# Optimization experiments

Measured on AMD Instinct MI355X. Metric: run time of the kernel, lower is better.

## Reference

```python
import jax, jax.numpy as jnp
import numpy as np

B, S, DIM = 32, 1, 4096
N_HEADS, N_KV, HD = 32, 8, 128
N_REP = N_HEADS // N_KV
MAX_SEQ = 2048


def _rope(x, cos, sin):
    # x: [b, s, h, d]; cos/sin: [s, d//2]; rotate consecutive pairs
    x2 = x.reshape(*x.shape[:-1], HD // 2, 2)
    x0, x1 = x2[..., 0], x2[..., 1]
    c = cos[None, :, None, :]
    s = sin[None, :, None, :]
    o0 = x0 * c - x1 * s
    o1 = x0 * s + x1 * c
    return jnp.stack([o0, o1], axis=-1).reshape(x.shape)


def setup_inputs() -> dict:
    key = jax.random.key(0)
    ks = jax.random.split(key, 9)
    start_pos = 2047
    # true RoPE frequencies at position start_pos
    inv_freq = 1.0 / (10000.0 ** (np.arange(0, HD, 2, dtype=np.float32) / HD))
    ang = (start_pos * inv_freq).astype(np.float32)[None, :]  # [1, HD//2]
    return {
        "x": jax.random.normal(ks[0], (B, S, DIM), jnp.float32),
        "freqs_cos": jnp.asarray(np.cos(ang)),
        "freqs_sin": jnp.asarray(np.sin(ang)),
        "wq": jax.random.normal(ks[1], (DIM, DIM), jnp.float32) * 0.02,
        "wk": jax.random.normal(ks[2], (N_KV * HD, DIM), jnp.float32) * 0.02,
        "wv": jax.random.normal(ks[3], (N_KV * HD, DIM), jnp.float32) * 0.02,
        "wo": jax.random.normal(ks[4], (DIM, DIM), jnp.float32) * 0.02,
        "cache_k": jax.random.normal(ks[5], (B, MAX_SEQ, N_KV, HD), jnp.float32),
        "cache_v": jax.random.normal(ks[6], (B, MAX_SEQ, N_KV, HD), jnp.float32),
        "start_pos": start_pos,
    }


def reference(x, freqs_cos, freqs_sin, wq, wk, wv, wo, cache_k, cache_v, start_pos):
    b, s, dim = x.shape  # s == 1 (decode)
    xq = (x @ wq.T).reshape(b, s, N_HEADS, HD)
    xk = (x @ wk.T).reshape(b, s, N_KV, HD)
    xv = (x @ wv.T).reshape(b, s, N_KV, HD)
    xq = _rope(xq, freqs_cos, freqs_sin)
    xk = _rope(xk, freqs_cos, freqs_sin)
    # KV-cache scatter write at start_pos
    cache_k = jax.lax.dynamic_update_slice(cache_k, xk, (0, start_pos, 0, 0))
    cache_v = jax.lax.dynamic_update_slice(cache_v, xv, (0, start_pos, 0, 0))
    t = start_pos + s
    keys = cache_k[:, :t]    # [b, t, kv, hd]
    values = cache_v[:, :t]  # [b, t, kv, hd]
    # GQA: group query heads over kv heads (no repeat_kv materialization)
    q = xq[:, 0].reshape(b, N_KV, N_REP, HD)  # [b, kv, rep, hd]
    scale = HD ** -0.5
    attn = jnp.einsum("bkrd,btkd->bkrt", q, keys) * scale  # [b, kv, rep, t]
    attn = jax.nn.softmax(attn.astype(jnp.float32), axis=-1).astype(q.dtype)
    out = jnp.einsum("bkrt,btkd->bkrd", attn, values).reshape(b, s, dim)
    return out @ wo.T
```

## Files before the change

kernel.cpp:

```cpp
#include <hip/hip_runtime.h>
#include <math.h>

#define B_ 32
#define DIM_ 4096
#define NKV_ 8
#define HD_ 128
#define T_ 2048
#define KS_ 16
#define QKV_ROWS_ 6144
#define O_ROWS_ 4096
#define NCHUNK_ 16
#define NSPLITW_ 64

#define Q_OFF    0
#define KNEW_OFF (Q_OFF + B_*DIM_)
#define VNEW_OFF (KNEW_OFF + B_*NKV_*HD_)
#define AO_OFF   (VNEW_OFF + B_*NKV_*HD_)
#define PQKV_OFF (AO_OFF + B_*DIM_)
#define PO_OFF   (PQKV_OFF + KS_*QKV_ROWS_*B_)
#define OPART_OFF (PO_OFF + KS_*O_ROWS_*B_)
#define ML_OFF   (OPART_OFF + B_*NKV_*NSPLITW_*4*HD_)

__device__ __forceinline__ void fma4(float4& a, const float4& x, float w) {
    a.x = fmaf(x.x, w, a.x); a.y = fmaf(x.y, w, a.y);
    a.z = fmaf(x.z, w, a.z); a.w = fmaf(x.w, w, a.w);
}

template<int NROWS>
__global__ __launch_bounds__(256) void gemm_split(
    const float* __restrict__ X, const float* __restrict__ W0,
    const float* __restrict__ W1, const float* __restrict__ W2,
    float* __restrict__ part)
{
    __shared__ float xs[32][36];
    __shared__ float wsh[32][132];
    const int rb = blockIdx.x, ks = blockIdx.y;
    const int row0 = rb * 128;
    const float* W; int wr0;
    if (NROWS == 4096 || row0 < 4096) { W = W0; wr0 = row0; }
    else if (row0 < 5120)             { W = W1; wr0 = row0 - 4096; }
    else                              { W = W2; wr0 = row0 - 5120; }
    const int tid = threadIdx.x;
    const int rt = tid & 31, bt = tid >> 5;
    float4 acc[4];
    acc[0] = acc[1] = acc[2] = acc[3] = make_float4(0.f,0.f,0.f,0.f);
    const int kc0 = ks * 256;
    const int xb = tid >> 3, xkq = tid & 7;
    float4 xpf, wpf[4];
    xpf = *(const float4*)(X + xb * DIM_ + kc0 + xkq * 4);
    #pragma unroll
    for (int j = 0; j < 4; ++j)
        wpf[j] = *(const float4*)(W + (wr0 + xb + 32*j) * DIM_ + kc0 + xkq * 4);
    for (int kt = 0; kt < 8; ++kt) {
        __syncthreads();
        xs[xkq*4+0][xb] = xpf.x; xs[xkq*4+1][xb] = xpf.y;
        xs[xkq*4+2][xb] = xpf.z; xs[xkq*4+3][xb] = xpf.w;
        #pragma unroll
        for (int j = 0; j < 4; ++j) {
            const int r = xb + 32*j;
            wsh[xkq*4+0][r] = wpf[j].x; wsh[xkq*4+1][r] = wpf[j].y;
            wsh[xkq*4+2][r] = wpf[j].z; wsh[xkq*4+3][r] = wpf[j].w;
        }
        __syncthreads();
        if (kt < 7) {
            const int kc = kc0 + (kt + 1) * 32;
            xpf = *(const float4*)(X + xb * DIM_ + kc + xkq * 4);
            #pragma unroll
            for (int j = 0; j < 4; ++j)
                wpf[j] = *(const float4*)(W + (wr0 + xb + 32*j) * DIM_ + kc + xkq * 4);
        }
        #pragma unroll
        for (int k = 0; k < 32; ++k) {
            float4 xv = *(const float4*)&xs[k][bt*4];
            float4 wv = *(const float4*)&wsh[k][rt*4];
            fma4(acc[0], xv, wv.x);
            fma4(acc[1], xv, wv.y);
            fma4(acc[2], xv, wv.z);
            fma4(acc[3], xv, wv.w);
        }
    }
    #pragma unroll
    for (int j = 0; j < 4; ++j) {
        const int row = row0 + rt * 4 + j;
        *(float4*)(part + (ks * NROWS + row) * 32 + bt * 4) = acc[j];
    }
}

__global__ __launch_bounds__(256) void reduce_rope(
    const float* __restrict__ part, const float* __restrict__ fc,
    const float* __restrict__ fs, float* __restrict__ qout,
    float* __restrict__ kout, float* __restrict__ vout)
{
    const int t = blockIdx.x * 256 + threadIdx.x;
    const int b = t & 31;
    const int row0 = (t >> 5) * 2;
    float s0 = 0.f, s1 = 0.f;
    #pragma unroll
    for (int ks = 0; ks < KS_; ++ks) {
        const float* p = part + (ks * QKV_ROWS_ + row0) * 32 + b;
        s0 += p[0];
        s1 += p[32];
    }
    if (row0 < 5120) {
        const int i = (row0 & 127) >> 1;
        const float c = fc[i], s = fs[i];
        const float o0 = s0 * c - s1 * s;
        const float o1 = s0 * s + s1 * c;
        if (row0 < 4096) {
            qout[b * 4096 + row0]     = o0;
            qout[b * 4096 + row0 + 1] = o1;
        } else {
            const int lr = row0 - 4096;
            kout[b * 1024 + lr]     = o0;
            kout[b * 1024 + lr + 1] = o1;
        }
    } else {
        const int lr = row0 - 5120;
        vout[b * 1024 + lr]     = s0;
        vout[b * 1024 + lr + 1] = s1;
    }
}

__global__ __launch_bounds__(256, 2) void attn_split(
    const float* __restrict__ q, const float* __restrict__ knew,
    const float* __restrict__ vnew, const float* __restrict__ ck,
    const float* __restrict__ cv, float* __restrict__ opart,
    float* __restrict__ ml)
{
    __shared__ float sct[4][32 * 33];
    const int chunk = blockIdx.x & 15;
    const int b     = blockIdx.x >> 4;
    const int tid = threadIdx.x;
    const int w  = tid >> 6, ln = tid & 63;
    const int kvl = ln >> 3, dsl = ln & 7;
    const int t0 = chunk * 128 + w * 32;
    const int split = chunk * 4 + w;
    const float scale = 0.08838834764831845f;
    float* ss = sct[w];

    float4 qr[4][4];
    #pragma unroll
    for (int r = 0; r < 4; ++r) {
        const float* qp = q + b * 4096 + (kvl * 4 + r) * 128 + dsl * 16;
        #pragma unroll
        for (int j = 0; j < 4; ++j) qr[r][j] = *(const float4*)(qp + j * 4);
    }
    const float* ckb = ck + (size_t)b * (2048 * 1024) + kvl * 128 + dsl * 16;
    const float* knb = knew + (b * 8 + kvl) * 128 + dsl * 16;

    for (int tt = 0; tt < 32; tt += 2) {
        float4 ka[2][4];
        #pragma unroll
        for (int u = 0; u < 2; ++u) {
            const int gt = t0 + tt + u;
            const float* kp = (gt == 2047) ? knb : (ckb + (size_t)gt * 1024);
            #pragma unroll
            for (int j = 0; j < 4; ++j) ka[u][j] = *(const float4*)(kp + j * 4);
        }
        #pragma unroll
        for (int u = 0; u < 2; ++u) {
            float d[4];
            #pragma unroll
            for (int r = 0; r < 4; ++r) {
                float s = 0.f;
                #pragma unroll
                for (int j = 0; j < 4; ++j) {
                    s = fmaf(ka[u][j].x, qr[r][j].x, s);
                    s = fmaf(ka[u][j].y, qr[r][j].y, s);
                    s = fmaf(ka[u][j].z, qr[r][j].z, s);
                    s = fmaf(ka[u][j].w, qr[r][j].w, s);
                }
                s += __shfl_xor(s, 1);
                s += __shfl_xor(s, 2);
                s += __shfl_xor(s, 4);
                d[r] = s * scale;
            }
            float out = d[0];
            const int dr = dsl & 3;
            if (dr == 1) out = d[1];
            if (dr == 2) out = d[2];
            if (dr == 3) out = d[3];
            if (dsl < 4) ss[(kvl * 4 + dsl) * 33 + tt + u] = out;
        }
    }
    __syncthreads();

    if (ln < 32) {
        float mx = -1e30f;
        #pragma unroll
        for (int t = 0; t < 32; ++t) mx = fmaxf(mx, ss[ln * 33 + t]);
        float sum = 0.f;
        #pragma unroll
        for (int t = 0; t < 32; ++t) {
            const float p = __expf(ss[ln * 33 + t] - mx);
            ss[ln * 33 + t] = p;
            sum += p;
        }
        const int kvp = ln >> 2, rp = ln & 3;
        *(float2*)(ml + (size_t)(((b * 8 + kvp) * 64 + split) * 4 + rp) * 2)
            = make_float2(mx, sum);
    }
    __syncthreads();

    float4 acc[4][4];
    #pragma unroll
    for (int r = 0; r < 4; ++r)
        #pragma unroll
        for (int j = 0; j < 4; ++j) acc[r][j] = make_float4(0.f,0.f,0.f,0.f);
    const float* cvb = cv + (size_t)b * (2048 * 1024) + kvl * 128 + dsl * 16;
    const float* vnb = vnew + (b * 8 + kvl) * 128 + dsl * 16;
    for (int tt = 0; tt < 32; tt += 2) {
        float4 va[2][4];
        #pragma unroll
        for (int u = 0; u < 2; ++u) {
            const int gt = t0 + tt + u;
            const float* vp = (gt == 2047) ? vnb : (cvb + (size_t)gt * 1024);
            #pragma unroll
            for (int j = 0; j < 4; ++j) va[u][j] = *(const float4*)(vp + j * 4);
        }
        #pragma unroll
        for (int u = 0; u < 2; ++u) {
            #pragma unroll
            for (int r = 0; r < 4; ++r) {
                const float p = ss[(kvl * 4 + r) * 33 + tt + u];
                #pragma unroll
                for (int j = 0; j < 4; ++j) fma4(acc[r][j], va[u][j], p);
            }
        }
    }
    float* ob = opart + (size_t)(((b * 8 + kvl) * 64 + split) * 4) * 128 + dsl * 16;
    #pragma unroll
    for (int r = 0; r < 4; ++r)
        #pragma unroll
        for (int j = 0; j < 4; ++j)
            *(float4*)(ob + r * 128 + j * 4) = acc[r][j];
}

__global__ __launch_bounds__(128) void attn_merge(
    const float* __restrict__ opart, const float* __restrict__ ml,
    float* __restrict__ ao)
{
    const int bk = blockIdx.x;
    const int tid = threadIdx.x;
    const int r = tid >> 5, dq = tid & 31;
    float M = -1e30f;
    #pragma unroll 8
    for (int sp = 0; sp < NSPLITW_; ++sp)
        M = fmaxf(M, ml[(size_t)((bk * 64 + sp) * 4 + r) * 2]);
    float L = 0.f;
    float4 o = make_float4(0.f, 0.f, 0.f, 0.f);
    #pragma unroll 4
    for (int sp = 0; sp < NSPLITW_; ++sp) {
        const float2 mlv = *(const float2*)(ml + (size_t)((bk * 64 + sp) * 4 + r) * 2);
        const float wgt = __expf(mlv.x - M);
        L += mlv.y * wgt;
        const float4 v = *(const float4*)(opart
            + (size_t)((bk * 64 + sp) * 4 + r) * 128 + dq * 4);
        fma4(o, v, wgt);
    }
    const float inv = 1.f / L;
    o.x *= inv; o.y *= inv; o.z *= inv; o.w *= inv;
    *(float4*)(ao + bk * 512 + r * 128 + dq * 4) = o;
}

__global__ __launch_bounds__(256) void reduce_out(
    const float* __restrict__ part, float* __restrict__ out)
{
    const int t = blockIdx.x * 256 + threadIdx.x;
    const int b = t & 31, row = t >> 5;
    float s = 0.f;
    #pragma unroll
    for (int ks = 0; ks < KS_; ++ks)
        s += part[(ks * O_ROWS_ + row) * 32 + b];
    out[b * 4096 + row] = s;
}

extern "C" void kernel_launch(void* const* d_in, const int* in_sizes, int n_in,
                              void* d_out, int out_size, void* d_ws, size_t ws_size,
                              hipStream_t stream)
{
    const float* x  = (const float*)d_in[0];
    const float* fc = (const float*)d_in[1];
    const float* fs = (const float*)d_in[2];
    const float* wq = (const float*)d_in[3];
    const float* wk = (const float*)d_in[4];
    const float* wv = (const float*)d_in[5];
    const float* wo = (const float*)d_in[6];
    const float* ck = (const float*)d_in[7];
    const float* cv = (const float*)d_in[8];
    float* ws    = (float*)d_ws;
    float* q     = ws + Q_OFF;
    float* knew  = ws + KNEW_OFF;
    float* vnew  = ws + VNEW_OFF;
    float* ao    = ws + AO_OFF;
    float* pqkv  = ws + PQKV_OFF;
    float* po    = ws + PO_OFF;
    float* opart = ws + OPART_OFF;
    float* mlp   = ws + ML_OFF;

    gemm_split<QKV_ROWS_><<<dim3(48, 16), 256, 0, stream>>>(x, wq, wk, wv, pqkv);
    reduce_rope<<<384, 256, 0, stream>>>(pqkv, fc, fs, q, knew, vnew);
    attn_split<<<512, 256, 0, stream>>>(q, knew, vnew, ck, cv, opart, mlp);
    attn_merge<<<256, 128, 0, stream>>>(opart, mlp, ao);
    gemm_split<O_ROWS_><<<dim3(32, 16), 256, 0, stream>>>(ao, wo, wo, wo, po);
    reduce_out<<<512, 256, 0, stream>>>(po, (float*)d_out);
}
```

Measured before the change: 670.2 us.

## Split attention blocks across KV-head halves to halve registers and raise occupancy

Each attention block now handles four KV heads instead of eight, with sixteen lanes per head each covering eight dimensions. This halves the per-thread query, key/value and accumulator registers. The grid doubles to 1024 blocks and launch bounds request four blocks per CU, to raise occupancy and memory-level parallelism on the KV cache stream. The softmax partial stage is reorganised into half-row pairs joined with a shuffle, and the dot-product reduction gains one more shuffle step.

```diff
diff --git a/kernel.cpp b/kernel.cpp
--- a/kernel.cpp
+++ b/kernel.cpp
@@ -9,7 +9,6 @@
 #define KS_ 16
 #define QKV_ROWS_ 6144
 #define O_ROWS_ 4096
-#define NCHUNK_ 16
 #define NSPLITW_ 64
 
 #define Q_OFF    0
@@ -121,119 +120,129 @@
     }
 }
 
-__global__ __launch_bounds__(256, 2) void attn_split(
+__global__ __launch_bounds__(256, 4) void attn_split(
     const float* __restrict__ q, const float* __restrict__ knew,
     const float* __restrict__ vnew, const float* __restrict__ ck,
     const float* __restrict__ cv, float* __restrict__ opart,
     float* __restrict__ ml)
 {
-    __shared__ float sct[4][32 * 33];
-    const int chunk = blockIdx.x & 15;
-    const int b     = blockIdx.x >> 4;
+    __shared__ float sct[4][16 * 33];
+    const int kvh   = blockIdx.x & 1;
+    const int chunk = (blockIdx.x >> 1) & 15;
+    const int b     = blockIdx.x >> 5;
     const int tid = threadIdx.x;
     const int w  = tid >> 6, ln = tid & 63;
-    const int kvl = ln >> 3, dsl = ln & 7;
+    const int kvl = ln >> 4, dsl = ln & 15;
+    const int kv  = kvh * 4 + kvl;
     const int t0 = chunk * 128 + w * 32;
     const int split = chunk * 4 + w;
     const float scale = 0.08838834764831845f;
     float* ss = sct[w];
 
-    float4 qr[4][4];
+    float4 qr[4][2];
     #pragma unroll
     for (int r = 0; r < 4; ++r) {
-        const float* qp = q + b * 4096 + (kvl * 4 + r) * 128 + dsl * 16;
-        #pragma unroll
-        for (int j = 0; j < 4; ++j) qr[r][j] = *(const float4*)(qp + j * 4);
-    }
-    const float* ckb = ck + (size_t)b * (2048 * 1024) + kvl * 128 + dsl * 16;
-    const float* knb = knew + (b * 8 + kvl) * 128 + dsl * 16;
-
-    for (int tt = 0; tt < 32; tt += 2) {
-        float4 ka[2][4];
-        #pragma unroll
-        for (int u = 0; u < 2; ++u) {
+        const float* qp = q + b * 4096 + (kv * 4 + r) * 128 + dsl * 8;
+        qr[r][0] = *(const float4*)qp;
+        qr[r][1] = *(const float4*)(qp + 4);
+    }
+    const float* ckb = ck + (size_t)b * (2048 * 1024) + kv * 128 + dsl * 8;
+    const float* knb = knew + (b * 8 + kv) * 128 + dsl * 8;
+
+    for (int tt = 0; tt < 32; tt += 4) {
+        float4 ka[4][2];
+        #pragma unroll
+        for (int u = 0; u < 4; ++u) {
             const int gt = t0 + tt + u;
             const float* kp = (gt == 2047) ? knb : (ckb + (size_t)gt * 1024);
-            #pragma unroll
-            for (int j = 0; j < 4; ++j) ka[u][j] = *(const float4*)(kp + j * 4);
-        }
-        #pragma unroll
-        for (int u = 0; u < 2; ++u) {
+            ka[u][0] = *(const float4*)kp;
+            ka[u][1] = *(const float4*)(kp + 4);
+        }
+        #pragma unroll
+        for (int u = 0; u < 4; ++u) {
             float d[4];
             #pragma unroll
             for (int r = 0; r < 4; ++r) {
                 float s = 0.f;
-                #pragma unroll
-                for (int j = 0; j < 4; ++j) {
-                    s = fmaf(ka[u][j].x, qr[r][j].x, s);
-                    s = fmaf(ka[u][j].y, qr[r][j].y, s);
-                    s = fmaf(ka[u][j].z, qr[r][j].z, s);
-                    s = fmaf(ka[u][j].w, qr[r][j].w, s);
-                }
+                s = fmaf(ka[u][0].x, qr[r][0].x, s);
+                s = fmaf(ka[u][0].y, qr[r][0].y, s);
+                s = fmaf(ka[u][0].z, qr[r][0].z, s);
+                s = fmaf(ka[u][0].w, qr[r][0].w, s);
+                s = fmaf(ka[u][1].x, qr[r][1].x, s);
+                s = fmaf(ka[u][1].y, qr[r][1].y, s);
+                s = fmaf(ka[u][1].z, qr[r][1].z, s);
+                s = fmaf(ka[u][1].w, qr[r][1].w, s);
                 s += __shfl_xor(s, 1);
                 s += __shfl_xor(s, 2);
                 s += __shfl_xor(s, 4);
+                s += __shfl_xor(s, 8);
                 d[r] = s * scale;
             }
             float out = d[0];
-            const int dr = dsl & 3;
-            if (dr == 1) out = d[1];
-            if (dr == 2) out = d[2];
-            if (dr == 3) out = d[3];
+            if (dsl == 1) out = d[1];
+            if (dsl == 2) out = d[2];
+            if (dsl == 3) out = d[3];
             if (dsl < 4) ss[(kvl * 4 + dsl) * 33 + tt + u] = out;
         }
     }
     __syncthreads();
 
     if (ln < 32) {
-        float mx = -1e30f;
-        #pragma unroll
-        for (int t = 0; t < 32; ++t) mx = fmaxf(mx, ss[ln * 33 + t]);
+        const int pr = ln >> 1, hf = ln & 1;
+        float* row = ss + pr * 33 + hf * 16;
+        float mx = row[0];
+        #pragma unroll
+        for (int t = 1; t < 16; ++t) mx = fmaxf(mx, row[t]);
+        mx = fmaxf(mx, __shfl_xor(mx, 1));
         float sum = 0.f;
         #pragma unroll
-        for (int t = 0; t < 32; ++t) {
-            const float p = __expf(ss[ln * 33 + t] - mx);
-            ss[ln * 33 + t] = p;
+        for (int t = 0; t < 16; ++t) {
+            const float p = __expf(row[t] - mx);
+            row[t] = p;
             sum += p;
         }
-        const int kvp = ln >> 2, rp = ln & 3;
-        *(float2*)(ml + (size_t)(((b * 8 + kvp) * 64 + split) * 4 + rp) * 2)
-            = make_float2(mx, sum);
+        sum += __shfl_xor(sum, 1);
+        if (hf == 0) {
+            const int kvg = kvh * 4 + (pr >> 2), rp = pr & 3;
+            *(float2*)(ml + (size_t)(((b * 8 + kvg) * 64 + split) * 4 + rp) * 2)
+                = make_float2(mx, sum);
+        }
     }
     __syncthreads();
 
-    float4 acc[4][4];
-    #pragma unroll
-    for (int r = 0; r < 4; ++r)
-        #pragma unroll
-        for (int j = 0; j < 4; ++j) acc[r][j] = make_float4(0.f,0.f,0.f,0.f);
-    const float* cvb = cv + (size_t)b * (2048 * 1024) + kvl * 128 + dsl * 16;
-    const float* vnb = vnew + (b * 8 + kvl) * 128 + dsl * 16;
-    for (int tt = 0; tt < 32; tt += 2) {
-        float4 va[2][4];
-        #pragma unroll
-        for (int u = 0; u < 2; ++u) {
+    float4 acc[4][2];
+    #pragma unroll
+    for (int r = 0; r < 4; ++r) {
+        acc[r][0] = make_float4(0.f,0.f,0.f,0.f);
+        acc[r][1] = make_float4(0.f,0.f,0.f,0.f);
+    }
+    const float* cvb = cv + (size_t)b * (2048 * 1024) + kv * 128 + dsl * 8;
+    const float* vnb = vnew + (b * 8 + kv) * 128 + dsl * 8;
+    for (int tt = 0; tt < 32; tt += 4) {
+        float4 va[4][2];
+        #pragma unroll
+        for (int u = 0; u < 4; ++u) {
             const int gt = t0 + tt + u;
             const float* vp = (gt == 2047) ? vnb : (cvb + (size_t)gt * 1024);
-            #pragma unroll
-            for (int j = 0; j < 4; ++j) va[u][j] = *(const float4*)(vp + j * 4);
-        }
-        #pragma unroll
-        for (int u = 0; u < 2; ++u) {
+            va[u][0] = *(const float4*)vp;
+            va[u][1] = *(const float4*)(vp + 4);
+        }
+        #pragma unroll
+        for (int u = 0; u < 4; ++u) {
             #pragma unroll
             for (int r = 0; r < 4; ++r) {
                 const float p = ss[(kvl * 4 + r) * 33 + tt + u];
-                #pragma unroll
-                for (int j = 0; j < 4; ++j) fma4(acc[r][j], va[u][j], p);
+                fma4(acc[r][0], va[u][0], p);
+                fma4(acc[r][1], va[u][1], p);
             }
         }
     }
-    float* ob = opart + (size_t)(((b * 8 + kvl) * 64 + split) * 4) * 128 + dsl * 16;
-    #pragma unroll
-    for (int r = 0; r < 4; ++r)
-        #pragma unroll
-        for (int j = 0; j < 4; ++j)
-            *(float4*)(ob + r * 128 + j * 4) = acc[r][j];
+    float* ob = opart + (size_t)(((b * 8 + kv) * 64 + split) * 4) * 128 + dsl * 8;
+    #pragma unroll
+    for (int r = 0; r < 4; ++r) {
+        *(float4*)(ob + r * 128)     = acc[r][0];
+        *(float4*)(ob + r * 128 + 4) = acc[r][1];
+    }
 }
 
 __global__ __launch_bounds__(128) void attn_merge(
@@ -300,7 +309,7 @@
 
     gemm_split<QKV_ROWS_><<<dim3(48, 16), 256, 0, stream>>>(x, wq, wk, wv, pqkv);
     reduce_rope<<<384, 256, 0, stream>>>(pqkv, fc, fs, q, knew, vnew);
-    attn_split<<<512, 256, 0, stream>>>(q, knew, vnew, ck, cv, opart, mlp);
+    attn_split<<<1024, 256, 0, stream>>>(q, knew, vnew, ck, cv, opart, mlp);
     attn_merge<<<256, 128, 0, stream>>>(opart, mlp, ao);
     gemm_split<O_ROWS_><<<dim3(32, 16), 256, 0, stream>>>(ao, wo, wo, wo, po);
     reduce_out<<<512, 256, 0, stream>>>(po, (float*)d_out);
```

After: 674.6 us. Within noise of the previous version (+0.7%).
